# Optimization experiments

Measured on AMD Instinct MI355X. Metric: run time of the kernel, lower is better.

Reference implementation:

```python
import jax, jax.numpy as jnp
import numpy as np

N = 4096
NUM_LIGHTS = 64
NUM_BOUNCES = 3          # fixed bounce count standing in for the MC walk solve
INV_FALLOFF_MAX = 1.0    # settings.inverse_falloff_max
MIN_DECAY = 1e-4         # settings.min_decay
EPS = 1e-8


def setup_inputs() -> dict:
    key = jax.random.key(0)
    ks = jax.random.split(key, 8)
    means3D = jax.random.normal(ks[0], (N, 3), jnp.float32) * 2.0
    geovalues = jax.random.uniform(ks[1], (N,), jnp.float32, 0.1, 1.0)
    scales = jax.random.uniform(ks[2], (N, 3), jnp.float32, 0.01, 0.05)
    rots = jax.random.normal(ks[3], (N, 4), jnp.float32)
    normals = jax.random.normal(ks[4], (N, 3), jnp.float32)
    normals = normals / jnp.linalg.norm(normals, axis=-1, keepdims=True)
    norm_factors = jax.random.uniform(ks[5], (N,), jnp.float32, 0.5, 1.5)
    emissions = jax.random.uniform(ks[6], (N, 3), jnp.float32)
    brdf_coeffs = jax.random.uniform(ks[7], (N, 3), jnp.float32, 0.0, 0.9)
    # light sources must be a contiguous tail block (see pl_indice slicing in source)
    is_light_source = jnp.arange(N) >= (N - NUM_LIGHTS)
    # non-light elements have zero emission; lights emit strongly
    emissions = jnp.where(is_light_source[:, None], emissions * 10.0, 0.0)
    return {"means3D": means3D, "geovalues": geovalues, "scales": scales,
            "rots": rots, "normals": normals, "norm_factors": norm_factors,
            "emissions": emissions, "brdf_coeffs": brdf_coeffs,
            "is_light_source": is_light_source}


def _form_factors(means3D, geovalues, scales, normals, norm_factors):
    # Pairwise point-to-disc form factors between Gaussian surfels.
    # diff[i,j] = direction from receiver i to emitter j
    diff = means3D[None, :, :] - means3D[:, None, :]            # [N,N,3]
    d2 = jnp.sum(diff * diff, axis=-1) + EPS                    # [N,N]
    inv_d = jax.lax.rsqrt(d2)
    cos_i = jax.nn.relu(jnp.einsum('ijk,ik->ij', diff, normals) * inv_d)
    cos_j = jax.nn.relu(-jnp.einsum('ijk,jk->ij', diff, normals) * inv_d)
    # clamped inverse-square light decay (inverse_falloff_max / min_decay)
    falloff = jnp.clip(1.0 / d2, MIN_DECAY, INV_FALLOFF_MAX)
    # emitter effective area ~ pi * s0 * s1, modulated by opacity & SH norm factor
    area_j = jnp.pi * scales[:, 0] * scales[:, 1] * geovalues * norm_factors
    F = cos_i * cos_j * falloff * (area_j[None, :] / jnp.pi)
    # no self-transport
    F = F * (1.0 - jnp.eye(F.shape[0], dtype=F.dtype))
    return F                                                    # [N,N]


def reference(means3D, geovalues, scales, rots, normals, norm_factors,
              emissions, brdf_coeffs, is_light_source):
    # NOTE: rots parameterize surfel orientation in the CUDA estimator; the
    # reference uses supplied normals directly (rots carried for API parity).
    F = _form_factors(means3D, geovalues, scales, normals, norm_factors)

    def bounce(B, _):
        gathered = jnp.einsum('ij,jc->ic', F, B)                # [N,3] transport
        B_new = emissions + brdf_coeffs * gathered
        # light sources only emit (decay_light_source handled in falloff)
        B_new = jnp.where(is_light_source[:, None], emissions, B_new)
        return B_new, None

    B0 = emissions
    B, _ = jax.lax.scan(bounce, B0, None, length=NUM_BOUNCES)
    # 'luminance' channel clamp: non-negative radiosity
    return jax.nn.relu(B)
```

## Files before the change

### kernel.cpp

```cpp
#include <hip/hip_runtime.h>

#define N 4096
#define NUM_LIGHTS 64
#define NRG 16
#define NSLICE 64
#define SLICE 64
#define EPSF 1e-8f
#define MIN_DECAY 1e-4f
#define INV_FALLOFF_MAX 1.0f


__device__ __forceinline__ float formfactor(float4 e1, float4 e2, float px,
                                            float py, float pz, float nx,
                                            float ny, float nz) {
  float dx = e1.x - px, dy = e1.y - py, dz = e1.z - pz;
  float d2 = fmaf(dx, dx, fmaf(dy, dy, fmaf(dz, dz, EPSF)));
  float inv = __builtin_amdgcn_rcpf(d2);
  float fall = fminf(fmaxf(inv, MIN_DECAY), INV_FALLOFF_MAX);
  float di = fmaf(dx, nx, fmaf(dy, ny, dz * nz));
  float dj = fmaf(dx, e2.x, fmaf(dy, e2.y, dz * e2.z));
  return fmaxf(di, 0.f) * fmaxf(-dj, 0.f) * inv * fall * e1.w;
}

__global__ __launch_bounds__(256) void bounce1_kernel(
    const float* __restrict__ means, const float* __restrict__ geo,
    const float* __restrict__ scales, const float* __restrict__ normals,
    const float* __restrict__ nf, const float* __restrict__ emis,
    const float* __restrict__ brdf, float4* __restrict__ B1,
    float* __restrict__ B2, float* __restrict__ out) {
  __shared__ float4 Em[NUM_LIGHTS], En[NUM_LIGHTS], Bs[NUM_LIGHTS];
  const int tid = threadIdx.x;
  const int i = blockIdx.x * 256 + tid;
  if (tid < NUM_LIGHTS) {
    int j = N - NUM_LIGHTS + tid;
    float aeff = scales[3 * j + 0] * scales[3 * j + 1] * geo[j] * nf[j];
    Em[tid] = make_float4(means[3 * j + 0], means[3 * j + 1], means[3 * j + 2], aeff);
    En[tid] = make_float4(normals[3 * j + 0], normals[3 * j + 1], normals[3 * j + 2], 0.f);
    Bs[tid] = make_float4(emis[3 * j + 0], emis[3 * j + 1], emis[3 * j + 2], 0.f);
  }
  __syncthreads();
  const float px = means[3 * i + 0], py = means[3 * i + 1], pz = means[3 * i + 2];
  const float nx = normals[3 * i + 0], ny = normals[3 * i + 1], nz = normals[3 * i + 2];
  float ax = 0.f, ay = 0.f, az = 0.f;
#pragma unroll 8
  for (int jj = 0; jj < NUM_LIGHTS; ++jj) {
    float w = formfactor(Em[jj], En[jj], px, py, pz, nx, ny, nz);
    float4 eb = Bs[jj];
    ax = fmaf(w, eb.x, ax);
    ay = fmaf(w, eb.y, ay);
    az = fmaf(w, eb.z, az);
  }
  float ex = emis[3 * i + 0], ey = emis[3 * i + 1], ez = emis[3 * i + 2];
  float bx, by, bz;
  if (i >= N - NUM_LIGHTS) {
    bx = ex; by = ey; bz = ez;
  } else {
    bx = fmaf(brdf[3 * i + 0], ax, ex);
    by = fmaf(brdf[3 * i + 1], ay, ey);
    bz = fmaf(brdf[3 * i + 2], az, ez);
  }
  B1[i] = make_float4(bx, by, bz, 0.f);
  B2[3 * i + 0] = ex; B2[3 * i + 1] = ey; B2[3 * i + 2] = ez;
  out[3 * i + 0] = ex; out[3 * i + 1] = ey; out[3 * i + 2] = ez;
}

template <int LAST>
__global__ __launch_bounds__(256) void bounceN_kernel(
    const float* __restrict__ means, const float* __restrict__ geo,
    const float* __restrict__ scales, const float* __restrict__ normals,
    const float* __restrict__ nf, const float* __restrict__ brdf,
    const float4* __restrict__ Bin4, const float* __restrict__ Bin3,
    float* __restrict__ accum) {
  __shared__ float4 Em[SLICE], En[SLICE], Bs[SLICE];
  const int tid = threadIdx.x;
  const int rg = blockIdx.x;
  const int s = blockIdx.y;
  const int j0 = s * SLICE;
  const int i = rg * 256 + tid;
  if (tid < SLICE) {
    int j = j0 + tid;
    float aeff = scales[3 * j + 0] * scales[3 * j + 1] * geo[j] * nf[j];
    Em[tid] = make_float4(means[3 * j + 0], means[3 * j + 1], means[3 * j + 2], aeff);
    En[tid] = make_float4(normals[3 * j + 0], normals[3 * j + 1], normals[3 * j + 2], 0.f);
    if (LAST)
      Bs[tid] = make_float4(Bin3[3 * j + 0], Bin3[3 * j + 1], Bin3[3 * j + 2], 0.f);
    else
      Bs[tid] = Bin4[j];
  }
  __syncthreads();
  const float px = means[3 * i + 0], py = means[3 * i + 1], pz = means[3 * i + 2];
  const float nx = normals[3 * i + 0], ny = normals[3 * i + 1], nz = normals[3 * i + 2];
  float ax = 0.f, ay = 0.f, az = 0.f;
#pragma unroll 8
  for (int jj = 0; jj < SLICE; ++jj) {
    float w = formfactor(Em[jj], En[jj], px, py, pz, nx, ny, nz);
    float4 eb = Bs[jj];
    ax = fmaf(w, eb.x, ax);
    ay = fmaf(w, eb.y, ay);
    az = fmaf(w, eb.z, az);
  }
  if (i < N - NUM_LIGHTS) {
    atomicAdd(&accum[3 * i + 0], brdf[3 * i + 0] * ax);
    atomicAdd(&accum[3 * i + 1], brdf[3 * i + 1] * ay);
    atomicAdd(&accum[3 * i + 2], brdf[3 * i + 2] * az);
  }
}

extern "C" void kernel_launch(void* const* d_in, const int* in_sizes, int n_in,
                              void* d_out, int out_size, void* d_ws, size_t ws_size,
                              hipStream_t stream) {
  const float* means   = (const float*)d_in[0];
  const float* geo     = (const float*)d_in[1];
  const float* scales  = (const float*)d_in[2];
  const float* normals = (const float*)d_in[4];
  const float* nf      = (const float*)d_in[5];
  const float* emis    = (const float*)d_in[6];
  const float* brdf    = (const float*)d_in[7];
  float* out = (float*)d_out;

  char* ws = (char*)d_ws;
  float4* B1 = (float4*)ws;  ws += (size_t)N * 16;
  float*  B2 = (float*)ws;

  bounce1_kernel<<<NRG, 256, 0, stream>>>(means, geo, scales, normals, nf,
                                          emis, brdf, B1, B2, out);
  dim3 grid(NRG, NSLICE);
  bounceN_kernel<0><<<grid, 256, 0, stream>>>(means, geo, scales, normals, nf,
                                              brdf, B1, nullptr, B2);
  bounceN_kernel<1><<<grid, 256, 0, stream>>>(means, geo, scales, normals, nf,
                                              brdf, nullptr, B2, out);
}
```

Measured before the change: 105.8 us.

## Fuse three bounce kernels into one cooperative kernel with grid syncs

Replaces the three separate launches with a single cooperative kernel of 256 blocks of 512 threads that uses grid.sync between bounces. Bounce 1 now uses a warp per receiver with shuffle reductions. The emitter area is pre-multiplied into the stored radiosity (B*area), so the tiles no longer hold it and the inner loop drops one multiply. Emitter position and normal tiles are loaded once and reused across both later bounces. The goal is to remove launch gaps and redundant loads, at the cost of cooperative-launch grid barriers and a larger block size.

```diff
diff --git a/kernel.cpp b/kernel.cpp
--- a/kernel.cpp
+++ b/kernel.cpp
@@ -1,108 +1,140 @@
 #include <hip/hip_runtime.h>
+#include <hip/hip_cooperative_groups.h>
+
+namespace cg = cooperative_groups;
 
 #define N 4096
 #define NUM_LIGHTS 64
-#define NRG 16
-#define NSLICE 64
-#define SLICE 64
+#define NTHR 512
+#define NRG 8
+#define SLICE 128
+#define NSLICE 32
+#define NBLK (NRG * NSLICE)
 #define EPSF 1e-8f
 #define MIN_DECAY 1e-4f
 #define INV_FALLOFF_MAX 1.0f
 
-
-__device__ __forceinline__ float formfactor(float4 e1, float4 e2, float px,
-                                            float py, float pz, float nx,
-                                            float ny, float nz) {
-  float dx = e1.x - px, dy = e1.y - py, dz = e1.z - pz;
+__device__ __forceinline__ float ffw(float ex, float ey, float ez,
+                                     float jx, float jy, float jz,
+                                     float px, float py, float pz,
+                                     float nx, float ny, float nz) {
+  float dx = ex - px, dy = ey - py, dz = ez - pz;
   float d2 = fmaf(dx, dx, fmaf(dy, dy, fmaf(dz, dz, EPSF)));
   float inv = __builtin_amdgcn_rcpf(d2);
   float fall = fminf(fmaxf(inv, MIN_DECAY), INV_FALLOFF_MAX);
   float di = fmaf(dx, nx, fmaf(dy, ny, dz * nz));
-  float dj = fmaf(dx, e2.x, fmaf(dy, e2.y, dz * e2.z));
-  return fmaxf(di, 0.f) * fmaxf(-dj, 0.f) * inv * fall * e1.w;
+  float dj = fmaf(dx, jx, fmaf(dy, jy, dz * jz));
+  return fmaxf(di, 0.f) * fmaxf(-dj, 0.f) * (inv * fall);
 }
 
-__global__ __launch_bounds__(256) void bounce1_kernel(
+__global__ __launch_bounds__(NTHR) void radiosity_fused(
     const float* __restrict__ means, const float* __restrict__ geo,
     const float* __restrict__ scales, const float* __restrict__ normals,
     const float* __restrict__ nf, const float* __restrict__ emis,
-    const float* __restrict__ brdf, float4* __restrict__ B1,
-    float* __restrict__ B2, float* __restrict__ out) {
-  __shared__ float4 Em[NUM_LIGHTS], En[NUM_LIGHTS], Bs[NUM_LIGHTS];
-  const int tid = threadIdx.x;
-  const int i = blockIdx.x * 256 + tid;
-  if (tid < NUM_LIGHTS) {
-    int j = N - NUM_LIGHTS + tid;
-    float aeff = scales[3 * j + 0] * scales[3 * j + 1] * geo[j] * nf[j];
-    Em[tid] = make_float4(means[3 * j + 0], means[3 * j + 1], means[3 * j + 2], aeff);
-    En[tid] = make_float4(normals[3 * j + 0], normals[3 * j + 1], normals[3 * j + 2], 0.f);
-    Bs[tid] = make_float4(emis[3 * j + 0], emis[3 * j + 1], emis[3 * j + 2], 0.f);
+    const float* __restrict__ brdf, float4* __restrict__ B1a,
+    float4* __restrict__ B2a, float* __restrict__ out) {
+  cg::grid_group grid = cg::this_grid();
+  __shared__ float4 Em[SLICE], En[SLICE], Bs[SLICE];
+
+  const int t = threadIdx.x;
+  const int b = blockIdx.x;
+
+  {
+    const int r = b * 16 + (t >> 5);
+    const int lane = t & 31;
+    const float px = means[3 * r], py = means[3 * r + 1], pz = means[3 * r + 2];
+    const float nx = normals[3 * r], ny = normals[3 * r + 1], nz = normals[3 * r + 2];
+    float ax = 0.f, ay = 0.f, az = 0.f;
+#pragma unroll
+    for (int k = 0; k < 2; ++k) {
+      int j = N - NUM_LIGHTS + lane + 32 * k;
+      float aeff = scales[3 * j] * scales[3 * j + 1] * geo[j] * nf[j];
+      float w = ffw(means[3 * j], means[3 * j + 1], means[3 * j + 2],
+                    normals[3 * j], normals[3 * j + 1], normals[3 * j + 2],
+                    px, py, pz, nx, ny, nz) * aeff;
+      ax = fmaf(w, emis[3 * j], ax);
+      ay = fmaf(w, emis[3 * j + 1], ay);
+      az = fmaf(w, emis[3 * j + 2], az);
+    }
+#pragma unroll
+    for (int m = 16; m >= 1; m >>= 1) {
+      ax += __shfl_xor(ax, m);
+      ay += __shfl_xor(ay, m);
+      az += __shfl_xor(az, m);
+    }
+    if (lane == 0) {
+      float ex = emis[3 * r], ey = emis[3 * r + 1], ez = emis[3 * r + 2];
+      float ar = scales[3 * r] * scales[3 * r + 1] * geo[r] * nf[r];
+      float bx, by, bz;
+      if (r >= N - NUM_LIGHTS) {
+        bx = ex; by = ey; bz = ez;
+      } else {
+        bx = fmaf(brdf[3 * r], ax, ex);
+        by = fmaf(brdf[3 * r + 1], ay, ey);
+        bz = fmaf(brdf[3 * r + 2], az, ez);
+      }
+      B1a[r] = make_float4(ar * bx, ar * by, ar * bz, 0.f);
+      B2a[r] = make_float4(ar * ex, ar * ey, ar * ez, 0.f);
+      out[3 * r] = ex; out[3 * r + 1] = ey; out[3 * r + 2] = ez;
+    }
   }
+
+  const int rg = b >> 5;
+  const int s = b & (NSLICE - 1);
+  const int j0 = s * SLICE;
+  const int i = rg * NTHR + t;
+  const float px = means[3 * i], py = means[3 * i + 1], pz = means[3 * i + 2];
+  const float nx = normals[3 * i], ny = normals[3 * i + 1], nz = normals[3 * i + 2];
+  const bool recv = (i < N - NUM_LIGHTS);
+  const float rbx = brdf[3 * i], rby = brdf[3 * i + 1], rbz = brdf[3 * i + 2];
+  const float ai = scales[3 * i] * scales[3 * i + 1] * geo[i] * nf[i];
+
+  if (t < SLICE) {
+    int j = j0 + t;
+    Em[t] = make_float4(means[3 * j], means[3 * j + 1], means[3 * j + 2], 0.f);
+  } else if (t < 2 * SLICE) {
+    int j = j0 + t - SLICE;
+    En[t - SLICE] = make_float4(normals[3 * j], normals[3 * j + 1], normals[3 * j + 2], 0.f);
+  }
+
+  grid.sync();
+
+  if (t >= 2 * SLICE && t < 3 * SLICE) Bs[t - 2 * SLICE] = B1a[j0 + t - 2 * SLICE];
   __syncthreads();
-  const float px = means[3 * i + 0], py = means[3 * i + 1], pz = means[3 * i + 2];
-  const float nx = normals[3 * i + 0], ny = normals[3 * i + 1], nz = normals[3 * i + 2];
+
   float ax = 0.f, ay = 0.f, az = 0.f;
 #pragma unroll 8
-  for (int jj = 0; jj < NUM_LIGHTS; ++jj) {
-    float w = formfactor(Em[jj], En[jj], px, py, pz, nx, ny, nz);
-    float4 eb = Bs[jj];
+  for (int jj = 0; jj < SLICE; ++jj) {
+    float4 em = Em[jj], en = En[jj], eb = Bs[jj];
+    float w = ffw(em.x, em.y, em.z, en.x, en.y, en.z, px, py, pz, nx, ny, nz);
     ax = fmaf(w, eb.x, ax);
     ay = fmaf(w, eb.y, ay);
     az = fmaf(w, eb.z, az);
   }
-  float ex = emis[3 * i + 0], ey = emis[3 * i + 1], ez = emis[3 * i + 2];
-  float bx, by, bz;
-  if (i >= N - NUM_LIGHTS) {
-    bx = ex; by = ey; bz = ez;
-  } else {
-    bx = fmaf(brdf[3 * i + 0], ax, ex);
-    by = fmaf(brdf[3 * i + 1], ay, ey);
-    bz = fmaf(brdf[3 * i + 2], az, ez);
+  if (recv) {
+    atomicAdd(&B2a[i].x, ai * rbx * ax);
+    atomicAdd(&B2a[i].y, ai * rby * ay);
+    atomicAdd(&B2a[i].z, ai * rbz * az);
   }
-  B1[i] = make_float4(bx, by, bz, 0.f);
-  B2[3 * i + 0] = ex; B2[3 * i + 1] = ey; B2[3 * i + 2] = ez;
-  out[3 * i + 0] = ex; out[3 * i + 1] = ey; out[3 * i + 2] = ez;
-}
 
-template <int LAST>
-__global__ __launch_bounds__(256) void bounceN_kernel(
-    const float* __restrict__ means, const float* __restrict__ geo,
-    const float* __restrict__ scales, const float* __restrict__ normals,
-    const float* __restrict__ nf, const float* __restrict__ brdf,
-    const float4* __restrict__ Bin4, const float* __restrict__ Bin3,
-    float* __restrict__ accum) {
-  __shared__ float4 Em[SLICE], En[SLICE], Bs[SLICE];
-  const int tid = threadIdx.x;
-  const int rg = blockIdx.x;
-  const int s = blockIdx.y;
-  const int j0 = s * SLICE;
-  const int i = rg * 256 + tid;
-  if (tid < SLICE) {
-    int j = j0 + tid;
-    float aeff = scales[3 * j + 0] * scales[3 * j + 1] * geo[j] * nf[j];
-    Em[tid] = make_float4(means[3 * j + 0], means[3 * j + 1], means[3 * j + 2], aeff);
-    En[tid] = make_float4(normals[3 * j + 0], normals[3 * j + 1], normals[3 * j + 2], 0.f);
-    if (LAST)
-      Bs[tid] = make_float4(Bin3[3 * j + 0], Bin3[3 * j + 1], Bin3[3 * j + 2], 0.f);
-    else
-      Bs[tid] = Bin4[j];
-  }
+  grid.sync();
+
+  if (t < SLICE) Bs[t] = B2a[j0 + t];
   __syncthreads();
-  const float px = means[3 * i + 0], py = means[3 * i + 1], pz = means[3 * i + 2];
-  const float nx = normals[3 * i + 0], ny = normals[3 * i + 1], nz = normals[3 * i + 2];
-  float ax = 0.f, ay = 0.f, az = 0.f;
+
+  ax = 0.f; ay = 0.f; az = 0.f;
 #pragma unroll 8
   for (int jj = 0; jj < SLICE; ++jj) {
-    float w = formfactor(Em[jj], En[jj], px, py, pz, nx, ny, nz);
-    float4 eb = Bs[jj];
+    float4 em = Em[jj], en = En[jj], eb = Bs[jj];
+    float w = ffw(em.x, em.y, em.z, en.x, en.y, en.z, px, py, pz, nx, ny, nz);
     ax = fmaf(w, eb.x, ax);
     ay = fmaf(w, eb.y, ay);
     az = fmaf(w, eb.z, az);
   }
-  if (i < N - NUM_LIGHTS) {
-    atomicAdd(&accum[3 * i + 0], brdf[3 * i + 0] * ax);
-    atomicAdd(&accum[3 * i + 1], brdf[3 * i + 1] * ay);
-    atomicAdd(&accum[3 * i + 2], brdf[3 * i + 2] * az);
+  if (recv) {
+    atomicAdd(&out[3 * i], rbx * ax);
+    atomicAdd(&out[3 * i + 1], rby * ay);
+    atomicAdd(&out[3 * i + 2], rbz * az);
   }
 }
 
@@ -119,14 +151,12 @@
   float* out = (float*)d_out;
 
   char* ws = (char*)d_ws;
-  float4* B1 = (float4*)ws;  ws += (size_t)N * 16;
-  float*  B2 = (float*)ws;
+  float4* B1a = (float4*)ws;
+  float4* B2a = (float4*)(ws + (size_t)N * 16);
 
-  bounce1_kernel<<<NRG, 256, 0, stream>>>(means, geo, scales, normals, nf,
-                                          emis, brdf, B1, B2, out);
-  dim3 grid(NRG, NSLICE);
-  bounceN_kernel<0><<<grid, 256, 0, stream>>>(means, geo, scales, normals, nf,
-                                              brdf, B1, nullptr, B2);
-  bounceN_kernel<1><<<grid, 256, 0, stream>>>(means, geo, scales, normals, nf,
-                                              brdf, nullptr, B2, out);
+  void* args[] = {(void*)&means, (void*)&geo, (void*)&scales, (void*)&normals,
+                  (void*)&nf,    (void*)&emis, (void*)&brdf,  (void*)&B1a,
+                  (void*)&B2a,   (void*)&out};
+  hipLaunchCooperativeKernel(reinterpret_cast<void*>(radiosity_fused),
+                             dim3(NBLK), dim3(NTHR), args, 0, stream);
 }
```

Result: slower. 173.9 us (+64.3%).
